# Kernel optimization log

Measured on AMD Instinct MI355X. Metric: run time of the kernel, lower is better.

Reference implementation:

```python
import jax, jax.numpy as jnp
import numpy as np
import math

B, C, H, W = 8, 512, 32, 32
NH = 8           # num_heads
G = 32           # group norm groups
EPS = 1e-6


def group_norm(x, gamma, beta, groups=G, eps=EPS):
    # x: [B, C, H, W]
    b, c, h, w = x.shape
    xr = x.reshape(b, groups, c // groups, h, w)
    mu = xr.mean(axis=(2, 3, 4), keepdims=True)
    var = xr.var(axis=(2, 3, 4), keepdims=True)
    xn = ((xr - mu) * jax.lax.rsqrt(var + eps)).reshape(b, c, h, w)
    return xn * gamma[None, :, None, None] + beta[None, :, None, None]


def conv2d(x, w, b, pad):
    y = jax.lax.conv_general_dilated(
        x, w, window_strides=(1, 1), padding=[(pad, pad), (pad, pad)],
        dimension_numbers=("NCHW", "OIHW", "NCHW"))
    return y + b[None, :, None, None]


def setup_inputs() -> dict:
    key = jax.random.key(0)
    ks = jax.random.split(key, 20)
    def n(k, shape, s=0.02):
        return jax.random.normal(k, shape, dtype=jnp.float32) * s
    f32 = jnp.float32
    return {
        "hidden_states": jax.random.normal(ks[0], (B, C, H, W), dtype=f32),
        "pre_g": jnp.ones(C, f32), "pre_b": jnp.zeros(C, f32),
        "norm_g": jnp.ones(C, f32), "norm_b": jnp.zeros(C, f32),
        "post_g": jnp.ones(C, f32), "post_b": jnp.zeros(C, f32),
        "pos_emb": n(ks[1], (1, C, 32, 32)),
        "wq": n(ks[2], (C, C)), "wk": n(ks[3], (C, C)), "wv": n(ks[4], (C, C)),
        "wq0": n(ks[5], (C // 2, C)), "wq1": n(ks[6], (C // 2, C)),
        "wk0": n(ks[7], (C // 2, C)), "wk1": n(ks[8], (C // 2, C)),
        "wv0": n(ks[9], (C // 2, C)), "wv1": n(ks[10], (C // 2, C)),
        "sa_w1": n(ks[11], (C // 8, C, 1, 1)), "sa_b1": jnp.zeros(C // 8, f32),
        "sa_w2": n(ks[12], (C // 8, C // 8, 3, 3)), "sa_b2": jnp.zeros(C // 8, f32),
        "sa_w3": n(ks[13], (1, C // 8, 1, 1)), "sa_b3": jnp.zeros(1, f32),
        "ff_w1": n(ks[14], (C, 2 * C)), "ff_b1": jnp.zeros(C, f32),
        "ff_w2": n(ks[15], (C, C)), "ff_b2": jnp.zeros(C, f32),
        "out_w": n(ks[16], (C, C)), "out_b": jnp.zeros(C, f32),
    }


def reference(hidden_states, pre_g, pre_b, norm_g, norm_b, post_g, post_b,
              pos_emb, wq, wk, wv, wq0, wq1, wk0, wk1, wv0, wv1,
              sa_w1, sa_b1, sa_w2, sa_b2, sa_w3, sa_b3,
              ff_w1, ff_b1, ff_w2, ff_b2, out_w, out_b):
    b, c, h, w = hidden_states.shape
    S = h * w
    residual = hidden_states
    x = group_norm(hidden_states, pre_g, pre_b)
    # H == W == 32: bilinear interpolation of pos_emb to its own size is identity
    x = x + pos_emb
    # conv-based sigmoid spatial gate
    s1 = jax.nn.silu(conv2d(x, sa_w1, sa_b1, 0))
    s2 = jax.nn.silu(conv2d(s1, sa_w2, sa_b2, 1))
    spatial_weights = jax.nn.sigmoid(conv2d(s2, sa_w3, sa_b3, 0))  # [B,1,H,W]
    spatial_enhanced = x * spatial_weights
    # standard attention path (self-attention: encoder states = normed tokens)
    sh = group_norm(x, norm_g, norm_b).reshape(b, c, S).transpose(0, 2, 1)  # [B,S,C]
    enc = sh
    hd = c // NH
    def split_heads(t):
        return t.reshape(b, S, NH, hd).transpose(0, 2, 1, 3)  # [B,NH,S,hd]
    qh = split_heads(sh @ wq.T)
    kh = split_heads(enc @ wk.T)
    vh = split_heads(enc @ wv.T)
    scores = jnp.einsum("bhqd,bhkd->bhqk", qh, kh) / math.sqrt(hd)
    probs = jax.nn.softmax(scores, axis=-1)
    standard_out = jnp.einsum("bhqk,bhkd->bhqd", probs, vh)
    standard_out = standard_out.transpose(0, 2, 1, 3).reshape(b, S, c)
    # multi-scale attention paths over the spatially gated features (single head)
    msh = spatial_enhanced.reshape(b, c, S).transpose(0, 2, 1)  # [B,S,C]
    parts = []
    for wqm, wkm, wvm in ((wq0, wk0, wv0), (wq1, wk1, wv1)):
        qm = msh @ wqm.T      # [B,S,C/2]
        km = enc @ wkm.T
        vm = enc @ wvm.T
        sc = jnp.einsum("bqd,bkd->bqk", qm, km) / math.sqrt(qm.shape[-1])
        parts.append(jnp.einsum("bqk,bkd->bqd", jax.nn.softmax(sc, axis=-1), vm))
    multi_out = jnp.concatenate(parts, axis=-1)            # [B,S,C]
    combined = jnp.concatenate([standard_out, multi_out], axis=-1)  # [B,S,2C]
    fused = jax.nn.silu(combined @ ff_w1.T + ff_b1) @ ff_w2.T + ff_b2  # dropout = eval
    final = fused @ out_w.T + out_b
    final = final.transpose(0, 2, 1).reshape(b, c, h, w)
    final = group_norm(final, post_g, post_b)
    return final + residual
```

## Files before the change

### kernel.cpp

```cpp
#include <hip/hip_runtime.h>

typedef unsigned short u16;
typedef unsigned long long u64;
typedef __attribute__((ext_vector_type(8))) short s8v;
typedef __attribute__((ext_vector_type(4))) short s4v;
typedef __attribute__((ext_vector_type(4))) float f4v;

#define LOG2E 1.4426950408889634f

__device__ __forceinline__ float b2f(u16 u) {
  union { unsigned u; float f; } x; x.u = ((unsigned)u) << 16; return x.f;
}
__device__ __forceinline__ u16 f2b(float f) {
  union { float f; unsigned u; } x; x.f = f;
  unsigned r = x.u + 0x7fffu + ((x.u >> 16) & 1u);
  return (u16)(r >> 16);
}
__device__ __forceinline__ unsigned cvtpk(float lo, float hi) {
  unsigned r;
  asm("v_cvt_pk_bf16_f32 %0, %1, %2" : "=v"(r) : "v"(lo), "v"(hi));
  return r;
}

#define MFMA16(a, b, c) __builtin_amdgcn_mfma_f32_16x16x32_bf16((a), (b), (c), 0, 0, 0)

__device__ __forceinline__ void gload16(const void* g, void* l) {
  __builtin_amdgcn_global_load_lds(
      (const __attribute__((address_space(1))) unsigned*)g,
      (__attribute__((address_space(3))) unsigned*)l, 16, 0, 0);
}

struct Segs {
  const float* src[14];
  int cum[15];
  float scl[14];
};

__global__ __launch_bounds__(256) void castk(Segs sg, u16* __restrict__ dst) {
  int gid = (blockIdx.x * 256 + threadIdx.x) * 4;
  if (gid >= sg.cum[14]) return;
  int s = 0;
  while (gid >= sg.cum[s + 1]) ++s;
  const float* sp = sg.src[s] + (gid - sg.cum[s]);
  float sc = sg.scl[s];
  f4v v = *(const f4v*)sp;
  s4v o;
  o[0] = (short)f2b(v[0] * sc); o[1] = (short)f2b(v[1] * sc);
  o[2] = (short)f2b(v[2] * sc); o[3] = (short)f2b(v[3] * sc);
  *(s4v*)(dst + gid) = o;
}

__global__ __launch_bounds__(256) void gn1_k(
    const float* __restrict__ hs, const float* __restrict__ pg, const float* __restrict__ pb,
    const float* __restrict__ pos, float* __restrict__ x,
    float* __restrict__ mu2, float* __restrict__ rs2)
{
  int bid = blockIdx.x;
  int b = bid >> 5, g = bid & 31;
  int tid = threadIdx.x, l = tid & 63, w = tid >> 6;
  const float* src = hs + ((size_t)b * 512 + g * 16) * 1024;
  const float* pp = pos + (size_t)(g * 16) * 1024;
  float* dst = x + ((size_t)b * 512 + g * 16) * 1024;
  f4v vals[16];
  float sum = 0.f, sq = 0.f;
#pragma unroll
  for (int i = 0; i < 16; ++i) {
    int idx = tid + i * 256;
    vals[i] = *(const f4v*)(src + (size_t)idx * 4);
    f4v v = vals[i];
    sum += v[0] + v[1] + v[2] + v[3];
    sq += v[0] * v[0] + v[1] * v[1] + v[2] * v[2] + v[3] * v[3];
  }
  __shared__ float red[8];
#pragma unroll
  for (int off = 1; off < 64; off <<= 1) { sum += __shfl_xor(sum, off); sq += __shfl_xor(sq, off); }
  if (l == 0) { red[w * 2] = sum; red[w * 2 + 1] = sq; }
  __syncthreads();
  float S = red[0] + red[2] + red[4] + red[6];
  float Q = red[1] + red[3] + red[5] + red[7];
  float mean = S * (1.f / 16384.f);
  float var = Q * (1.f / 16384.f) - mean * mean;
  float rstd = rsqrtf(var + 1e-6f);
  __syncthreads();
  float sum2 = 0.f, sq2 = 0.f;
#pragma unroll
  for (int i = 0; i < 16; ++i) {
    int idx = tid + i * 256;
    int c = idx >> 8;
    float gam = pg[g * 16 + c], bet = pb[g * 16 + c];
    f4v v = vals[i];
    f4v pe = *(const f4v*)(pp + (size_t)idx * 4);
    f4v o;
#pragma unroll
    for (int j = 0; j < 4; ++j) o[j] = (v[j] - mean) * rstd * gam + bet + pe[j];
    *(f4v*)(dst + (size_t)idx * 4) = o;
    sum2 += o[0] + o[1] + o[2] + o[3];
    sq2 += o[0] * o[0] + o[1] * o[1] + o[2] * o[2] + o[3] * o[3];
  }
#pragma unroll
  for (int off = 1; off < 64; off <<= 1) { sum2 += __shfl_xor(sum2, off); sq2 += __shfl_xor(sq2, off); }
  if (l == 0) { red[w * 2] = sum2; red[w * 2 + 1] = sq2; }
  __syncthreads();
  if (tid == 0) {
    float S2 = red[0] + red[2] + red[4] + red[6];
    float Q2 = red[1] + red[3] + red[5] + red[7];
    float m2 = S2 * (1.f / 16384.f);
    float v2 = Q2 * (1.f / 16384.f) - m2 * m2;
    mu2[b * 32 + g] = m2;
    rs2[b * 32 + g] = rsqrtf(v2 + 1e-6f);
  }
}

__global__ __launch_bounds__(256) void trans_gn2(
    const float* __restrict__ x, const float* __restrict__ mu2, const float* __restrict__ rs2,
    const float* __restrict__ ng, const float* __restrict__ nb,
    u16* __restrict__ xt, u16* __restrict__ sh)
{
  __shared__ float lds[512 * 17];
  int st = blockIdx.x, b = blockIdx.y;
  int tid = threadIdx.x;
  const float* xp = x + (size_t)b * 512 * 1024 + st * 16;
#pragma unroll
  for (int i = 0; i < 8; ++i) {
    int idx = tid + i * 256;
    int c = idx >> 2, sq = idx & 3;
    f4v v = *(const f4v*)(xp + (size_t)c * 1024 + sq * 4);
#pragma unroll
    for (int j = 0; j < 4; ++j) lds[c * 17 + sq * 4 + j] = v[j];
  }
  __syncthreads();
  int s = tid & 15, cb0 = (tid >> 4) * 32;
  size_t token = (size_t)b * 1024 + st * 16 + s;
  float m0 = mu2[b * 32 + (cb0 >> 4)], m1 = mu2[b * 32 + (cb0 >> 4) + 1];
  float r0 = rs2[b * 32 + (cb0 >> 4)], r1 = rs2[b * 32 + (cb0 >> 4) + 1];
#pragma unroll
  for (int q = 0; q < 4; ++q) {
    s8v ox, os;
#pragma unroll
    for (int j = 0; j < 8; ++j) {
      int cj = q * 8 + j;
      int c = cb0 + cj;
      float v = lds[c * 17 + s];
      ox[j] = (short)f2b(v);
      float mm = (cj < 16) ? m0 : m1;
      float rr = (cj < 16) ? r0 : r1;
      os[j] = (short)f2b((v - mm) * rr * ng[c] + nb[c]);
    }
    *(s8v*)(xt + token * 512 + cb0 + q * 8) = ox;
    *(s8v*)(sh + token * 512 + cb0 + q * 8) = os;
  }
}

template <int BM, int BN, bool SILU, bool OUT32, bool BIAS>
__global__ __launch_bounds__(256, 2) void gemm_k(
    const u16* __restrict__ A, int lda,
    const u16* __restrict__ Bw, int ldb,
    void* __restrict__ Cp, int ldc,
    const float* __restrict__ bias, int K, int ntx)
{
  constexpr int WMT = BM / 2, WNT = BN / 2, MF = WMT / 16, NF = WNT / 16;
  __shared__ u16 Al[BM * 64];
  __shared__ u16 Bl[BN * 64];
  const int tid = threadIdx.x, l = tid & 63, w = tid >> 6;
  const int lg = l >> 4, lr = l & 15;
  const int wm = w >> 1, wn = w & 1;
  const int flat = blockIdx.x;
  const int cpx = gridDim.x >> 3;
  const int id = (flat & 7) * cpx + (flat >> 3);
  const int nt = id % ntx, mt = id / ntx;
  const u16* Ag = A + (size_t)mt * BM * lda;
  const u16* Bg = Bw + (size_t)nt * BN * ldb;
  const f4v z = {0.f, 0.f, 0.f, 0.f};
  f4v acc[MF][NF];
#pragma unroll
  for (int i = 0; i < MF; ++i)
#pragma unroll
    for (int j = 0; j < NF; ++j) acc[i][j] = z;

  for (int kt = 0; kt < K; kt += 64) {
    __syncthreads();
    for (int f = tid; f < BM * 8; f += 256) {
      int row = f >> 3, g = (f & 7) ^ (row & 7);
      gload16(Ag + (size_t)row * lda + kt + g * 8, (char*)Al + f * 16);
    }
    for (int f = tid; f < BN * 8; f += 256) {
      int row = f >> 3, g = (f & 7) ^ (row & 7);
      gload16(Bg + (size_t)row * ldb + kt + g * 8, (char*)Bl + f * 16);
    }
    __syncthreads();
#pragma unroll
    for (int ks = 0; ks < 2; ++ks) {
      s8v af[MF], bf[NF];
#pragma unroll
      for (int mf = 0; mf < MF; ++mf) {
        int row = wm * WMT + mf * 16 + lr;
        af[mf] = *(const s8v*)((const char*)Al + row * 128 + (((ks * 4 + lg) ^ (row & 7)) << 4));
      }
#pragma unroll
      for (int nf = 0; nf < NF; ++nf) {
        int row = wn * WNT + nf * 16 + lr;
        bf[nf] = *(const s8v*)((const char*)Bl + row * 128 + (((ks * 4 + lg) ^ (row & 7)) << 4));
      }
#pragma unroll
      for (int mf = 0; mf < MF; ++mf)
#pragma unroll
        for (int nf = 0; nf < NF; ++nf)
          acc[mf][nf] = MFMA16(af[mf], bf[nf], acc[mf][nf]);
    }
  }
#pragma unroll
  for (int mf = 0; mf < MF; ++mf) {
    int row0 = mt * BM + wm * WMT + mf * 16 + lg * 4;
#pragma unroll
    for (int nf = 0; nf < NF; ++nf) {
      int col = nt * BN + wn * WNT + nf * 16 + lr;
      float bv = BIAS ? bias[col] : 0.f;
#pragma unroll
      for (int r = 0; r < 4; ++r) {
        float v = acc[mf][nf][r] + bv;
        if (SILU) v = v / (1.f + exp2f(-v * LOG2E));
        size_t off = (size_t)(row0 + r) * ldc + col;
        if (OUT32) ((float*)Cp)[off] = v;
        else ((u16*)Cp)[off] = f2b(v);
      }
    }
  }
}

__global__ __launch_bounds__(256) void im2col_k(const u16* __restrict__ s1t, u16* __restrict__ col) {
  int gid = blockIdx.x * 256 + threadIdx.x;
  if (gid >= 8192 * 64) return;
  int token = gid >> 6, c = gid & 63;
  int s = token & 1023, y = s >> 5, xx = s & 31;
  u16* dst = col + (size_t)token * 576 + c * 9;
#pragma unroll
  for (int dy = 0; dy < 3; ++dy)
#pragma unroll
    for (int dx = 0; dx < 3; ++dx) {
      int yy = y + dy - 1, x2 = xx + dx - 1;
      u16 v = 0;
      if (yy >= 0 && yy < 32 && x2 >= 0 && x2 < 32)
        v = s1t[(size_t)(token + (dy - 1) * 32 + (dx - 1)) * 64 + c];
      dst[dy * 3 + dx] = v;
    }
}

__global__ __launch_bounds__(256) void conv3_k(
    const u16* __restrict__ s2t, const float* __restrict__ w3,
    const float* __restrict__ b3, float* __restrict__ gate)
{
  int token = blockIdx.x * 256 + threadIdx.x;
  if (token >= 8192) return;
  float acc = b3[0];
#pragma unroll
  for (int q = 0; q < 8; ++q) {
    s8v v = *(const s8v*)(s2t + (size_t)token * 64 + q * 8);
#pragma unroll
    for (int e = 0; e < 8; ++e) acc += b2f((u16)v[e]) * w3[q * 8 + e];
  }
  gate[token] = 1.f / (1.f + exp2f(-acc * LOG2E));
}

__global__ __launch_bounds__(256) void mshk(
    const u16* __restrict__ xt, const float* __restrict__ gate, u16* __restrict__ msh)
{
  int gid = blockIdx.x * 256 + threadIdx.x;
  if (gid >= 8192 * 64) return;
  int token = gid >> 6, j = gid & 63;
  float gt = gate[token];
  s8v v = *(const s8v*)(xt + (size_t)token * 512 + j * 8);
  s8v o;
#pragma unroll
  for (int e = 0; e < 8; ++e) o[e] = (short)f2b(b2f((u16)v[e]) * gt);
  *(s8v*)(msh + (size_t)token * 512 + j * 8) = o;
}

template <int HD>
__global__ __launch_bounds__(256) void tv_k(const u16* __restrict__ proj, int col0,
                                            u16* __restrict__ out)
{
  __shared__ u16 tile[64][HD + 2];
  const int tid = threadIdx.x;
  const int kb = blockIdx.x, y = blockIdx.y;
  const int nh = 512 / HD;
  const int b = y / nh, hh = y % nh;
  const u16* src = proj + ((size_t)b * 1024 + kb * 64) * 2560 + col0 + hh * HD;
  for (int f = tid; f < 64 * HD / 8; f += 256) {
    int key = f / (HD / 8), c = f % (HD / 8);
    *(s8v*)&tile[key][c * 8] = *(const s8v*)(src + (size_t)key * 2560 + c * 8);
  }
  __syncthreads();
  u16* dst = out + (size_t)y * HD * 1024 + kb * 64;
  for (int idx = tid; idx < HD * 16; idx += 256) {
    int d = idx >> 4, a = idx & 15;
    u16 e0 = tile[a][d], e1 = tile[16 + a][d], e2 = tile[32 + a][d], e3 = tile[48 + a][d];
    u64 v = (u64)e0 | ((u64)e1 << 16) | ((u64)e2 << 32) | ((u64)e3 << 48);
    *(u64*)(dst + (size_t)d * 1024 + a * 4) = v;
  }
}

__global__ __launch_bounds__(256, 4) void attn_std(
    const u16* __restrict__ proj, const u16* __restrict__ vts, u16* __restrict__ comb)
{
  const int tid = threadIdx.x, l = tid & 63, w = tid >> 6;
  const int lg = l >> 4, lr = l & 15;
  const int flat = blockIdx.x;
  const int xcd = flat & 7, idx = flat >> 3;
  const int bh = xcd + 8 * (idx >> 4);
  const int qt = idx & 15;
  const int b = bh >> 3, h = bh & 7;
  const size_t tokb = (size_t)b * 1024;
  __shared__ u16 Kl[64 * 64];
  __shared__ u16 Vl[64 * 64];
  __shared__ u16 Pl[4][16 * 64];
  const int qr0 = qt * 64 + w * 16;
  s8v qf[2];
#pragma unroll
  for (int ks = 0; ks < 2; ++ks)
    qf[ks] = *(const s8v*)(proj + (tokb + qr0 + lr) * 2560 + h * 64 + ks * 32 + lg * 8);
  const f4v z = {0.f, 0.f, 0.f, 0.f};
  f4v acc[4];
  float lsl[4] = {0.f, 0.f, 0.f, 0.f};
#pragma unroll
  for (int r = 0; r < 4; ++r) acc[r] = z;
  const u16* vbase = vts + (size_t)bh * 64 * 1024;

  for (int kt = 0; kt < 16; ++kt) {
    __syncthreads();
    for (int f = tid; f < 512; f += 256) {
      int key = f >> 3, g = (f & 7) ^ (key & 7);
      gload16(proj + (tokb + kt * 64 + key) * 2560 + 512 + h * 64 + g * 8, (char*)Kl + f * 16);
    }
    for (int f = tid; f < 512; f += 256) {
      int d = f >> 3, c = (f & 7) ^ (d & 7);
      gload16(vbase + (size_t)d * 1024 + kt * 64 + c * 8, (char*)Vl + f * 16);
    }
    __syncthreads();
    f4v sf[4];
#pragma unroll
    for (int nf = 0; nf < 4; ++nf) sf[nf] = z;
#pragma unroll
    for (int ks = 0; ks < 2; ++ks) {
      s8v kfr[4];
#pragma unroll
      for (int nf = 0; nf < 4; ++nf) {
        int row = nf * 16 + lr;
        kfr[nf] = *(const s8v*)((const char*)Kl + row * 128 + (((ks * 4 + lg) ^ (row & 7)) << 4));
      }
#pragma unroll
      for (int nf = 0; nf < 4; ++nf) sf[nf] = MFMA16(qf[ks], kfr[nf], sf[nf]);
    }
#pragma unroll
    for (int r = 0; r < 4; ++r) {
      float pv[4];
#pragma unroll
      for (int nf = 0; nf < 4; ++nf) pv[nf] = exp2f(sf[nf][r]);
      lsl[r] += (pv[0] + pv[1]) + (pv[2] + pv[3]);
      int q = lg * 4 + r;
      u64 pk = (u64)cvtpk(pv[0], pv[1]) | ((u64)cvtpk(pv[2], pv[3]) << 32);
      *(u64*)((char*)&Pl[w][0] + q * 128 + ((((lr >> 1) ^ (q & 7)) << 4)) + (lr & 1) * 8) = pk;
    }
#pragma unroll
    for (int ks2 = 0; ks2 < 2; ++ks2) {
      int g = ks2 * 4 + lg;
      s8v pfr = *(const s8v*)((const char*)&Pl[w][0] + lr * 128 + ((g ^ (lr & 7)) << 4));
#pragma unroll
      for (int nf = 0; nf < 4; ++nf) {
        int d = nf * 16 + lr;
        s8v vfr = *(const s8v*)((const char*)Vl + d * 128 + ((g ^ (d & 7)) << 4));
        acc[nf] = MFMA16(pfr, vfr, acc[nf]);
      }
    }
  }
#pragma unroll
  for (int r = 0; r < 4; ++r) {
    float t = lsl[r];
#pragma unroll
    for (int off = 1; off < 16; off <<= 1) t += __shfl_xor(t, off);
    float inv = 1.f / t;
    size_t row = tokb + qr0 + lg * 4 + r;
#pragma unroll
    for (int nf = 0; nf < 4; ++nf)
      comb[row * 1024 + h * 64 + nf * 16 + lr] = f2b(acc[nf][r] * inv);
  }
}

__global__ __launch_bounds__(256, 2) void attn_ms(
    const u16* __restrict__ proj, const u16* __restrict__ qm, const u16* __restrict__ vtm,
    u16* __restrict__ pacc, float* __restrict__ pl)
{
  const int tid = threadIdx.x, l = tid & 63, w = tid >> 6;
  const int lg = l >> 4, lr = l & 15;
  const int flat = blockIdx.x;
  const int xcd = flat & 7, idx = flat >> 3;
  const int bp = xcd + 8 * (idx >> 5);
  const int rest = idx & 31;
  const int qt = rest >> 1, ks = rest & 1;
  const int b = bp >> 1, p = bp & 1;
  const size_t tokb = (size_t)b * 1024;
  __shared__ u16 Kl[64 * 256];
  __shared__ u16 Vl[256 * 64];
  __shared__ u16 Pl[4][16 * 64];
  const int qr0 = qt * 64 + w * 16;
  s8v qf[8];
#pragma unroll
  for (int kf = 0; kf < 8; ++kf)
    qf[kf] = *(const s8v*)(qm + (tokb + qr0 + lr) * 512 + p * 256 + kf * 32 + lg * 8);
  const f4v z = {0.f, 0.f, 0.f, 0.f};
  f4v acc[16];
#pragma unroll
  for (int i = 0; i < 16; ++i) acc[i] = z;
  float lsl[4] = {0.f, 0.f, 0.f, 0.f};
  const u16* vbase = vtm + (size_t)bp * 256 * 1024;

  for (int kk = 0; kk < 8; ++kk) {
    const int key0 = ks * 512 + kk * 64;
    __syncthreads();
    for (int f = tid; f < 2048; f += 256) {
      int key = f >> 5, pgc = f & 31;
      int g = (pgc & 24) | ((pgc & 7) ^ (key & 7));
      gload16(proj + (tokb + key0 + key) * 2560 + 1536 + p * 256 + g * 8, (char*)Kl + f * 16);
    }
    for (int f = tid; f < 2048; f += 256) {
      int d = f >> 3, c = (f & 7) ^ (d & 7);
      gload16(vbase + (size_t)d * 1024 + key0 + c * 8, (char*)Vl + f * 16);
    }
    __syncthreads();
    f4v sf[4];
#pragma unroll
    for (int nf = 0; nf < 4; ++nf) sf[nf] = z;
#pragma unroll
    for (int ksi = 0; ksi < 8; ++ksi) {
      s8v kfr[4];
#pragma unroll
      for (int nf = 0; nf < 4; ++nf) {
        int row = nf * 16 + lr;
        int g = ksi * 4 + lg;
        int pg2 = (g & 24) | ((g & 7) ^ (row & 7));
        kfr[nf] = *(const s8v*)((const char*)Kl + row * 512 + (pg2 << 4));
      }
#pragma unroll
      for (int nf = 0; nf < 4; ++nf) sf[nf] = MFMA16(qf[ksi], kfr[nf], sf[nf]);
    }
#pragma unroll
    for (int r = 0; r < 4; ++r) {
      float pv[4];
#pragma unroll
      for (int nf = 0; nf < 4; ++nf) pv[nf] = exp2f(sf[nf][r]);
      lsl[r] += (pv[0] + pv[1]) + (pv[2] + pv[3]);
      int q = lg * 4 + r;
      u64 pk = (u64)cvtpk(pv[0], pv[1]) | ((u64)cvtpk(pv[2], pv[3]) << 32);
      *(u64*)((char*)&Pl[w][0] + q * 128 + ((((lr >> 1) ^ (q & 7)) << 4)) + (lr & 1) * 8) = pk;
    }
#pragma unroll
    for (int ks2 = 0; ks2 < 2; ++ks2) {
      int g = ks2 * 4 + lg;
      s8v pfr = *(const s8v*)((const char*)&Pl[w][0] + lr * 128 + ((g ^ (lr & 7)) << 4));
#pragma unroll
      for (int nfd = 0; nfd < 16; ++nfd) {
        int d = nfd * 16 + lr;
        s8v vfr = *(const s8v*)((const char*)Vl + d * 128 + ((g ^ (d & 7)) << 4));
        acc[nfd] = MFMA16(pfr, vfr, acc[nfd]);
      }
    }
  }
#pragma unroll
  for (int r = 0; r < 4; ++r) {
    float t = lsl[r];
#pragma unroll
    for (int off = 1; off < 16; off <<= 1) t += __shfl_xor(t, off);
    size_t prow = ((size_t)(bp * 2 + ks) * 16 + qt) * 64 + w * 16 + lg * 4 + r;
#pragma unroll
    for (int nfd = 0; nfd < 16; ++nfd)
      pacc[prow * 256 + nfd * 16 + lr] = f2b(acc[nfd][r]);
    if (lr == 0) pl[prow] = t;
  }
}

__global__ __launch_bounds__(256) void ms_comb(
    const u16* __restrict__ pacc, const float* __restrict__ pl,
    u16* __restrict__ comb)
{
  const int qt = blockIdx.x, bp = blockIdx.y;
  const int tid = threadIdx.x;
  const int row = tid >> 2, seg = tid & 3;
  size_t prow0 = ((size_t)(bp * 2 + 0) * 16 + qt) * 64 + row;
  size_t prow1 = ((size_t)(bp * 2 + 1) * 16 + qt) * 64 + row;
  float inv = 1.f / (pl[prow0] + pl[prow1]);
  const int b = bp >> 1, p = bp & 1;
  size_t orow = ((size_t)b * 1024 + qt * 64 + row) * 1024 + 512 + p * 256 + seg * 64;
#pragma unroll
  for (int j = 0; j < 8; ++j) {
    s8v v0 = *(const s8v*)(pacc + prow0 * 256 + seg * 64 + j * 8);
    s8v v1 = *(const s8v*)(pacc + prow1 * 256 + seg * 64 + j * 8);
    s8v ov;
#pragma unroll
    for (int e = 0; e < 8; ++e)
      ov[e] = (short)f2b((b2f((u16)v0[e]) + b2f((u16)v1[e])) * inv);
    *(s8v*)(comb + orow + j * 8) = ov;
  }
}

__global__ __launch_bounds__(256) void gn3_stats(
    const float* __restrict__ fin, float* __restrict__ mu3, float* __restrict__ rs3)
{
  int bid = blockIdx.x;
  int b = bid >> 5, g = bid & 31;
  int tid = threadIdx.x, l = tid & 63, w = tid >> 6;
  const float* fp = fin + (size_t)b * 1024 * 512 + g * 16;
  float sum = 0.f, sq = 0.f;
#pragma unroll
  for (int i = 0; i < 16; ++i) {
    int idx = tid + i * 256;
    int s = idx >> 2, cq = idx & 3;
    f4v v = *(const f4v*)(fp + (size_t)s * 512 + cq * 4);
    sum += v[0] + v[1] + v[2] + v[3];
    sq += v[0] * v[0] + v[1] * v[1] + v[2] * v[2] + v[3] * v[3];
  }
  __shared__ float red[8];
#pragma unroll
  for (int off = 1; off < 64; off <<= 1) { sum += __shfl_xor(sum, off); sq += __shfl_xor(sq, off); }
  if (l == 0) { red[w * 2] = sum; red[w * 2 + 1] = sq; }
  __syncthreads();
  if (tid == 0) {
    float S = red[0] + red[2] + red[4] + red[6];
    float Q = red[1] + red[3] + red[5] + red[7];
    float mean = S * (1.f / 16384.f);
    float var = Q * (1.f / 16384.f) - mean * mean;
    mu3[b * 32 + g] = mean;
    rs3[b * 32 + g] = rsqrtf(var + 1e-6f);
  }
}

__global__ __launch_bounds__(256) void final_k(
    const float* __restrict__ fin, const float* __restrict__ mu3, const float* __restrict__ rs3,
    const float* __restrict__ postg, const float* __restrict__ postb,
    const float* __restrict__ res, float* __restrict__ out)
{
  __shared__ float lds[16 * 513];
  int st = blockIdx.x, b = blockIdx.y;
  int tid = threadIdx.x;
  const float* fp = fin + ((size_t)b * 1024 + st * 16) * 512;
#pragma unroll
  for (int i = 0; i < 8; ++i) {
    int idx = tid + i * 256;
    int s = idx >> 7, cq = idx & 127;
    f4v v = *(const f4v*)(fp + (size_t)s * 512 + cq * 4);
#pragma unroll
    for (int j = 0; j < 4; ++j) lds[s * 513 + cq * 4 + j] = v[j];
  }
  __syncthreads();
#pragma unroll
  for (int cc = 0; cc < 2; ++cc) {
    int c = tid * 2 + cc;
    int g = c >> 4;
    float m = mu3[b * 32 + g], rv = rs3[b * 32 + g];
    float ga = postg[c], be = postb[c];
    const float* rp = res + ((size_t)b * 512 + c) * 1024 + st * 16;
    float* op = out + ((size_t)b * 512 + c) * 1024 + st * 16;
#pragma unroll
    for (int q = 0; q < 4; ++q) {
      f4v rr = *(const f4v*)(rp + q * 4);
      f4v o;
#pragma unroll
      for (int j = 0; j < 4; ++j) {
        float v = lds[(q * 4 + j) * 513 + c];
        o[j] = (v - m) * rv * ga + be + rr[j];
      }
      *(f4v*)(op + q * 4) = o;
    }
  }
}

extern "C" void kernel_launch(void* const* d_in, const int* in_sizes, int n_in,
                              void* d_out, int out_size, void* d_ws, size_t ws_size,
                              hipStream_t stream) {
  (void)in_sizes; (void)n_in; (void)out_size; (void)ws_size;
  const float* hs     = (const float*)d_in[0];
  const float* pre_g  = (const float*)d_in[1];
  const float* pre_b  = (const float*)d_in[2];
  const float* norm_g = (const float*)d_in[3];
  const float* norm_b = (const float*)d_in[4];
  const float* post_g = (const float*)d_in[5];
  const float* post_b = (const float*)d_in[6];
  const float* pos    = (const float*)d_in[7];
  const float* sa_b1  = (const float*)d_in[18];
  const float* sa_b2  = (const float*)d_in[20];
  const float* sa_w3  = (const float*)d_in[21];
  const float* sa_b3  = (const float*)d_in[22];
  const float* ff_b1  = (const float*)d_in[24];
  const float* ff_b2  = (const float*)d_in[26];
  const float* out_b  = (const float*)d_in[28];

  char* ws = (char*)d_ws;
  size_t off = 0;
  auto alloc = [&](size_t bytes) -> void* {
    void* pp = ws + off;
    off += (bytes + 255) & ~(size_t)255;
    return pp;
  };
  float* x    = (float*)alloc((size_t)16777216);
  u16* sh     = (u16*)alloc((size_t)8388608);
  u16* xt     = (u16*)alloc((size_t)8388608);
  float* mu2  = (float*)alloc(1024);
  float* rs2  = (float*)alloc(1024);
  float* mu3  = (float*)alloc(1024);
  float* rs3  = (float*)alloc(1024);
  float* pl   = (float*)alloc(262144);
  u16* wcat   = (u16*)alloc((size_t)2691072 * 2);
  u16* proj   = (u16*)alloc((size_t)8192 * 2560 * 2);
  u16* qmb    = (u16*)alloc((size_t)8388608);
  u16* s1t    = (u16*)alloc((size_t)1048576);
  u16* colb   = (u16*)alloc((size_t)8192 * 576 * 2);
  u16* s2t    = (u16*)alloc((size_t)1048576);
  float* gate = (float*)alloc((size_t)32768);
  u16* msh    = (u16*)alloc((size_t)8388608);
  u16* comb   = (u16*)alloc((size_t)16777216);
  u16* f1     = (u16*)alloc((size_t)8388608);
  u16* f2     = (u16*)alloc((size_t)8388608);
  float* fin  = x;
  u16* pacc   = (u16*)x;
  u16* vts    = colb;
  u16* vtm    = msh;

  u16* Wbig = wcat;
  u16* Wq01 = wcat + 1310720;
  u16* W1   = wcat + 1572864;
  u16* W2   = wcat + 1605632;
  u16* Wff1 = wcat + 1642496;
  u16* Wff2 = wcat + 2166784;
  u16* Wout = wcat + 2428928;

  Segs sg;
  const int srcidx[14] = {8, 9, 10, 13, 14, 15, 16, 11, 12, 17, 19, 23, 25, 27};
  const int segsz[14] = {262144, 262144, 262144, 131072, 131072, 131072, 131072,
                         131072, 131072, 32768, 36864, 524288, 262144, 262144};
  int cum = 0;
  for (int i = 0; i < 14; ++i) {
    sg.src[i] = (const float*)d_in[srcidx[i]];
    sg.cum[i] = cum;
    sg.scl[i] = 1.f;
    cum += segsz[i];
  }
  sg.cum[14] = cum;
  sg.scl[0] = 0.125f * LOG2E;
  sg.scl[7] = 0.0625f * LOG2E;
  sg.scl[8] = 0.0625f * LOG2E;

  dim3 blk(256);
  castk<<<2628, blk, 0, stream>>>(sg, wcat);
  gn1_k<<<256, blk, 0, stream>>>(hs, pre_g, pre_b, pos, x, mu2, rs2);
  trans_gn2<<<dim3(64, 8), blk, 0, stream>>>(x, mu2, rs2, norm_g, norm_b, xt, sh);
  gemm_k<128, 128, false, false, false><<<1280, blk, 0, stream>>>(
      sh, 512, Wbig, 512, proj, 2560, nullptr, 512, 20);
  gemm_k<64, 64, true, false, true><<<128, blk, 0, stream>>>(
      xt, 512, W1, 512, s1t, 64, sa_b1, 512, 1);
  im2col_k<<<2048, blk, 0, stream>>>(s1t, colb);
  gemm_k<64, 64, true, false, true><<<128, blk, 0, stream>>>(
      colb, 576, W2, 576, s2t, 64, sa_b2, 576, 1);
  conv3_k<<<32, blk, 0, stream>>>(s2t, sa_w3, sa_b3, gate);
  mshk<<<2048, blk, 0, stream>>>(xt, gate, msh);
  gemm_k<128, 64, false, false, false><<<512, blk, 0, stream>>>(
      msh, 512, Wq01, 512, qmb, 512, nullptr, 512, 8);
  tv_k<64><<<dim3(16, 64), blk, 0, stream>>>(proj, 1024, vts);
  tv_k<256><<<dim3(16, 16), blk, 0, stream>>>(proj, 2048, vtm);
  attn_std<<<1024, blk, 0, stream>>>(proj, vts, comb);
  attn_ms<<<512, blk, 0, stream>>>(proj, qmb, vtm, pacc, pl);
  ms_comb<<<dim3(16, 16), blk, 0, stream>>>(pacc, pl, comb);
  gemm_k<128, 64, true, false, true><<<512, blk, 0, stream>>>(
      comb, 1024, Wff1, 1024, f1, 512, ff_b1, 1024, 8);
  gemm_k<128, 64, false, false, true><<<512, blk, 0, stream>>>(
      f1, 512, Wff2, 512, f2, 512, ff_b2, 512, 8);
  gemm_k<128, 64, false, true, true><<<512, blk, 0, stream>>>(
      f2, 512, Wout, 512, fin, 512, out_b, 512, 8);
  gn3_stats<<<256, blk, 0, stream>>>(fin, mu3, rs3);
  final_k<<<dim3(64, 8), blk, 0, stream>>>(fin, mu3, rs3, post_g, post_b, hs, (float*)d_out);
}
```

Measured before the change: 259.5 us.

## Double-buffer LDS tiles in GEMM and attention; read V fragments directly from global

```diff
diff --git a/kernel.cpp b/kernel.cpp
--- a/kernel.cpp
+++ b/kernel.cpp
@@ -159,8 +159,8 @@
     const float* __restrict__ bias, int K, int ntx)
 {
   constexpr int WMT = BM / 2, WNT = BN / 2, MF = WMT / 16, NF = WNT / 16;
-  __shared__ u16 Al[BM * 64];
-  __shared__ u16 Bl[BN * 64];
+  __shared__ u16 Al[2][BM * 64];
+  __shared__ u16 Bl[2][BN * 64];
   const int tid = threadIdx.x, l = tid & 63, w = tid >> 6;
   const int lg = l >> 4, lr = l & 15;
   const int wm = w >> 1, wn = w & 1;
@@ -177,29 +177,34 @@
 #pragma unroll
     for (int j = 0; j < NF; ++j) acc[i][j] = z;
 
-  for (int kt = 0; kt < K; kt += 64) {
-    __syncthreads();
+  auto stage = [&](int buf, int kt) {
     for (int f = tid; f < BM * 8; f += 256) {
       int row = f >> 3, g = (f & 7) ^ (row & 7);
-      gload16(Ag + (size_t)row * lda + kt + g * 8, (char*)Al + f * 16);
+      gload16(Ag + (size_t)row * lda + kt + g * 8, (char*)&Al[buf][0] + f * 16);
     }
     for (int f = tid; f < BN * 8; f += 256) {
       int row = f >> 3, g = (f & 7) ^ (row & 7);
-      gload16(Bg + (size_t)row * ldb + kt + g * 8, (char*)Bl + f * 16);
-    }
-    __syncthreads();
+      gload16(Bg + (size_t)row * ldb + kt + g * 8, (char*)&Bl[buf][0] + f * 16);
+    }
+  };
+
+  stage(0, 0);
+  __syncthreads();
+  int cur = 0;
+  for (int kt = 0; kt < K; kt += 64) {
+    if (kt + 64 < K) stage(cur ^ 1, kt + 64);
 #pragma unroll
     for (int ks = 0; ks < 2; ++ks) {
       s8v af[MF], bf[NF];
 #pragma unroll
       for (int mf = 0; mf < MF; ++mf) {
         int row = wm * WMT + mf * 16 + lr;
-        af[mf] = *(const s8v*)((const char*)Al + row * 128 + (((ks * 4 + lg) ^ (row & 7)) << 4));
+        af[mf] = *(const s8v*)((const char*)&Al[cur][0] + row * 128 + (((ks * 4 + lg) ^ (row & 7)) << 4));
       }
 #pragma unroll
       for (int nf = 0; nf < NF; ++nf) {
         int row = wn * WNT + nf * 16 + lr;
-        bf[nf] = *(const s8v*)((const char*)Bl + row * 128 + (((ks * 4 + lg) ^ (row & 7)) << 4));
+        bf[nf] = *(const s8v*)((const char*)&Bl[cur][0] + row * 128 + (((ks * 4 + lg) ^ (row & 7)) << 4));
       }
 #pragma unroll
       for (int mf = 0; mf < MF; ++mf)
@@ -207,6 +212,8 @@
         for (int nf = 0; nf < NF; ++nf)
           acc[mf][nf] = MFMA16(af[mf], bf[nf], acc[mf][nf]);
     }
+    __syncthreads();
+    cur ^= 1;
   }
 #pragma unroll
   for (int mf = 0; mf < MF; ++mf) {
@@ -310,8 +317,7 @@
   const int qt = idx & 15;
   const int b = bh >> 3, h = bh & 7;
   const size_t tokb = (size_t)b * 1024;
-  __shared__ u16 Kl[64 * 64];
-  __shared__ u16 Vl[64 * 64];
+  __shared__ u16 Kl[2][64 * 64];
   __shared__ u16 Pl[4][16 * 64];
   const int qr0 = qt * 64 + w * 16;
   s8v qf[2];
@@ -325,17 +331,19 @@
   for (int r = 0; r < 4; ++r) acc[r] = z;
   const u16* vbase = vts + (size_t)bh * 64 * 1024;
 
-  for (int kt = 0; kt < 16; ++kt) {
-    __syncthreads();
+  auto stageK = [&](int buf, int kt) {
     for (int f = tid; f < 512; f += 256) {
       int key = f >> 3, g = (f & 7) ^ (key & 7);
-      gload16(proj + (tokb + kt * 64 + key) * 2560 + 512 + h * 64 + g * 8, (char*)Kl + f * 16);
-    }
-    for (int f = tid; f < 512; f += 256) {
-      int d = f >> 3, c = (f & 7) ^ (d & 7);
-      gload16(vbase + (size_t)d * 1024 + kt * 64 + c * 8, (char*)Vl + f * 16);
-    }
-    __syncthreads();
+      gload16(proj + (tokb + kt * 64 + key) * 2560 + 512 + h * 64 + g * 8,
+              (char*)&Kl[buf][0] + f * 16);
+    }
+  };
+
+  stageK(0, 0);
+  __syncthreads();
+  int cur = 0;
+  for (int kt = 0; kt < 16; ++kt) {
+    if (kt < 15) stageK(cur ^ 1, kt + 1);
     f4v sf[4];
 #pragma unroll
     for (int nf = 0; nf < 4; ++nf) sf[nf] = z;
@@ -345,7 +353,7 @@
 #pragma unroll
       for (int nf = 0; nf < 4; ++nf) {
         int row = nf * 16 + lr;
-        kfr[nf] = *(const s8v*)((const char*)Kl + row * 128 + (((ks * 4 + lg) ^ (row & 7)) << 4));
+        kfr[nf] = *(const s8v*)((const char*)&Kl[cur][0] + row * 128 + (((ks * 4 + lg) ^ (row & 7)) << 4));
       }
 #pragma unroll
       for (int nf = 0; nf < 4; ++nf) sf[nf] = MFMA16(qf[ks], kfr[nf], sf[nf]);
@@ -366,11 +374,12 @@
       s8v pfr = *(const s8v*)((const char*)&Pl[w][0] + lr * 128 + ((g ^ (lr & 7)) << 4));
 #pragma unroll
       for (int nf = 0; nf < 4; ++nf) {
-        int d = nf * 16 + lr;
-        s8v vfr = *(const s8v*)((const char*)Vl + d * 128 + ((g ^ (d & 7)) << 4));
+        s8v vfr = *(const s8v*)(vbase + (size_t)(nf * 16 + lr) * 1024 + kt * 64 + g * 8);
         acc[nf] = MFMA16(pfr, vfr, acc[nf]);
       }
     }
+    __syncthreads();
+    cur ^= 1;
   }
 #pragma unroll
   for (int r = 0; r < 4; ++r) {
@@ -398,8 +407,7 @@
   const int qt = rest >> 1, ks = rest & 1;
   const int b = bp >> 1, p = bp & 1;
   const size_t tokb = (size_t)b * 1024;
-  __shared__ u16 Kl[64 * 256];
-  __shared__ u16 Vl[256 * 64];
+  __shared__ u16 Kl[2][64 * 256];
   __shared__ u16 Pl[4][16 * 64];
   const int qr0 = qt * 64 + w * 16;
   s8v qf[8];
@@ -412,20 +420,24 @@
   for (int i = 0; i < 16; ++i) acc[i] = z;
   float lsl[4] = {0.f, 0.f, 0.f, 0.f};
   const u16* vbase = vtm + (size_t)bp * 256 * 1024;
-
-  for (int kk = 0; kk < 8; ++kk) {
-    const int key0 = ks * 512 + kk * 64;
-    __syncthreads();
+  const int kbase = ks * 512;
+
+  auto stageK = [&](int buf, int kk) {
+    const int key0 = kbase + kk * 64;
     for (int f = tid; f < 2048; f += 256) {
       int key = f >> 5, pgc = f & 31;
       int g = (pgc & 24) | ((pgc & 7) ^ (key & 7));
-      gload16(proj + (tokb + key0 + key) * 2560 + 1536 + p * 256 + g * 8, (char*)Kl + f * 16);
-    }
-    for (int f = tid; f < 2048; f += 256) {
-      int d = f >> 3, c = (f & 7) ^ (d & 7);
-      gload16(vbase + (size_t)d * 1024 + key0 + c * 8, (char*)Vl + f * 16);
-    }
-    __syncthreads();
+      gload16(proj + (tokb + key0 + key) * 2560 + 1536 + p * 256 + g * 8,
+              (char*)&Kl[buf][0] + f * 16);
+    }
+  };
+
+  stageK(0, 0);
+  __syncthreads();
+  int cur = 0;
+  for (int kk = 0; kk < 8; ++kk) {
+    const int key0 = kbase + kk * 64;
+    if (kk < 7) stageK(cur ^ 1, kk + 1);
     f4v sf[4];
 #pragma unroll
     for (int nf = 0; nf < 4; ++nf) sf[nf] = z;
@@ -437,7 +449,7 @@
         int row = nf * 16 + lr;
         int g = ksi * 4 + lg;
         int pg2 = (g & 24) | ((g & 7) ^ (row & 7));
-        kfr[nf] = *(const s8v*)((const char*)Kl + row * 512 + (pg2 << 4));
+        kfr[nf] = *(const s8v*)((const char*)&Kl[cur][0] + row * 512 + (pg2 << 4));
       }
 #pragma unroll
       for (int nf = 0; nf < 4; ++nf) sf[nf] = MFMA16(qf[ksi], kfr[nf], sf[nf]);
@@ -458,11 +470,12 @@
       s8v pfr = *(const s8v*)((const char*)&Pl[w][0] + lr * 128 + ((g ^ (lr & 7)) << 4));
 #pragma unroll
       for (int nfd = 0; nfd < 16; ++nfd) {
-        int d = nfd * 16 + lr;
-        s8v vfr = *(const s8v*)((const char*)Vl + d * 128 + ((g ^ (d & 7)) << 4));
+        s8v vfr = *(const s8v*)(vbase + (size_t)(nfd * 16 + lr) * 1024 + key0 + g * 8);
         acc[nfd] = MFMA16(pfr, vfr, acc[nfd]);
       }
     }
+    __syncthreads();
+    cur ^= 1;
   }
 #pragma unroll
   for (int r = 0; r < 4; ++r) {
```

Result: slower. 334.1 us (+28.8%).

## Double-buffer LDS tiles in GEMM and standard attention kernels

Applied to the files above, without the earlier changes.

```diff
diff --git a/kernel.cpp b/kernel.cpp
--- a/kernel.cpp
+++ b/kernel.cpp
@@ -159,8 +159,8 @@
     const float* __restrict__ bias, int K, int ntx)
 {
   constexpr int WMT = BM / 2, WNT = BN / 2, MF = WMT / 16, NF = WNT / 16;
-  __shared__ u16 Al[BM * 64];
-  __shared__ u16 Bl[BN * 64];
+  __shared__ u16 Al[2][BM * 64];
+  __shared__ u16 Bl[2][BN * 64];
   const int tid = threadIdx.x, l = tid & 63, w = tid >> 6;
   const int lg = l >> 4, lr = l & 15;
   const int wm = w >> 1, wn = w & 1;
@@ -177,29 +177,34 @@
 #pragma unroll
     for (int j = 0; j < NF; ++j) acc[i][j] = z;
 
-  for (int kt = 0; kt < K; kt += 64) {
-    __syncthreads();
+  auto stage = [&](int buf, int kt) {
     for (int f = tid; f < BM * 8; f += 256) {
       int row = f >> 3, g = (f & 7) ^ (row & 7);
-      gload16(Ag + (size_t)row * lda + kt + g * 8, (char*)Al + f * 16);
+      gload16(Ag + (size_t)row * lda + kt + g * 8, (char*)&Al[buf][0] + f * 16);
     }
     for (int f = tid; f < BN * 8; f += 256) {
       int row = f >> 3, g = (f & 7) ^ (row & 7);
-      gload16(Bg + (size_t)row * ldb + kt + g * 8, (char*)Bl + f * 16);
-    }
-    __syncthreads();
+      gload16(Bg + (size_t)row * ldb + kt + g * 8, (char*)&Bl[buf][0] + f * 16);
+    }
+  };
+
+  stage(0, 0);
+  __syncthreads();
+  int cur = 0;
+  for (int kt = 0; kt < K; kt += 64) {
+    if (kt + 64 < K) stage(cur ^ 1, kt + 64);
 #pragma unroll
     for (int ks = 0; ks < 2; ++ks) {
       s8v af[MF], bf[NF];
 #pragma unroll
       for (int mf = 0; mf < MF; ++mf) {
         int row = wm * WMT + mf * 16 + lr;
-        af[mf] = *(const s8v*)((const char*)Al + row * 128 + (((ks * 4 + lg) ^ (row & 7)) << 4));
+        af[mf] = *(const s8v*)((const char*)&Al[cur][0] + row * 128 + (((ks * 4 + lg) ^ (row & 7)) << 4));
       }
 #pragma unroll
       for (int nf = 0; nf < NF; ++nf) {
         int row = wn * WNT + nf * 16 + lr;
-        bf[nf] = *(const s8v*)((const char*)Bl + row * 128 + (((ks * 4 + lg) ^ (row & 7)) << 4));
+        bf[nf] = *(const s8v*)((const char*)&Bl[cur][0] + row * 128 + (((ks * 4 + lg) ^ (row & 7)) << 4));
       }
 #pragma unroll
       for (int mf = 0; mf < MF; ++mf)
@@ -207,6 +212,8 @@
         for (int nf = 0; nf < NF; ++nf)
           acc[mf][nf] = MFMA16(af[mf], bf[nf], acc[mf][nf]);
     }
+    __syncthreads();
+    cur ^= 1;
   }
 #pragma unroll
   for (int mf = 0; mf < MF; ++mf) {
@@ -310,8 +317,8 @@
   const int qt = idx & 15;
   const int b = bh >> 3, h = bh & 7;
   const size_t tokb = (size_t)b * 1024;
-  __shared__ u16 Kl[64 * 64];
-  __shared__ u16 Vl[64 * 64];
+  __shared__ u16 Kl[2][64 * 64];
+  __shared__ u16 Vl[2][64 * 64];
   __shared__ u16 Pl[4][16 * 64];
   const int qr0 = qt * 64 + w * 16;
   s8v qf[2];
@@ -325,17 +332,23 @@
   for (int r = 0; r < 4; ++r) acc[r] = z;
   const u16* vbase = vts + (size_t)bh * 64 * 1024;
 
-  for (int kt = 0; kt < 16; ++kt) {
-    __syncthreads();
+  auto stage = [&](int buf, int kt) {
     for (int f = tid; f < 512; f += 256) {
       int key = f >> 3, g = (f & 7) ^ (key & 7);
-      gload16(proj + (tokb + kt * 64 + key) * 2560 + 512 + h * 64 + g * 8, (char*)Kl + f * 16);
+      gload16(proj + (tokb + kt * 64 + key) * 2560 + 512 + h * 64 + g * 8,
+              (char*)&Kl[buf][0] + f * 16);
     }
     for (int f = tid; f < 512; f += 256) {
       int d = f >> 3, c = (f & 7) ^ (d & 7);
-      gload16(vbase + (size_t)d * 1024 + kt * 64 + c * 8, (char*)Vl + f * 16);
-    }
-    __syncthreads();
+      gload16(vbase + (size_t)d * 1024 + kt * 64 + c * 8, (char*)&Vl[buf][0] + f * 16);
+    }
+  };
+
+  stage(0, 0);
+  __syncthreads();
+  int cur = 0;
+  for (int kt = 0; kt < 16; ++kt) {
+    if (kt < 15) stage(cur ^ 1, kt + 1);
     f4v sf[4];
 #pragma unroll
     for (int nf = 0; nf < 4; ++nf) sf[nf] = z;
@@ -345,7 +358,7 @@
 #pragma unroll
       for (int nf = 0; nf < 4; ++nf) {
         int row = nf * 16 + lr;
-        kfr[nf] = *(const s8v*)((const char*)Kl + row * 128 + (((ks * 4 + lg) ^ (row & 7)) << 4));
+        kfr[nf] = *(const s8v*)((const char*)&Kl[cur][0] + row * 128 + (((ks * 4 + lg) ^ (row & 7)) << 4));
       }
 #pragma unroll
       for (int nf = 0; nf < 4; ++nf) sf[nf] = MFMA16(qf[ks], kfr[nf], sf[nf]);
@@ -367,10 +380,12 @@
 #pragma unroll
       for (int nf = 0; nf < 4; ++nf) {
         int d = nf * 16 + lr;
-        s8v vfr = *(const s8v*)((const char*)Vl + d * 128 + ((g ^ (d & 7)) << 4));
+        s8v vfr = *(const s8v*)((const char*)&Vl[cur][0] + d * 128 + ((g ^ (d & 7)) << 4));
         acc[nf] = MFMA16(pfr, vfr, acc[nf]);
       }
     }
+    __syncthreads();
+    cur ^= 1;
   }
 #pragma unroll
   for (int r = 0; r < 4; ++r) {
```

Measured after the change: 261.7 us. No clear change (+0.9%).
